# Performance work log

Hardware: AMD Instinct MI355X
Metric: run time of the kernel (lower is better)

The kernel has to match this reference:

```python
import jax, jax.numpy as jnp
import numpy as np


def setup_inputs() -> dict:
    key = jax.random.key(0)
    k1, k2 = jax.random.split(key)
    B, C, H, W = 8, 128, 96, 160
    x1 = jax.random.normal(k1, (B, C, H, W), dtype=jnp.float32)
    x2 = jax.random.normal(k2, (B, C, H, W), dtype=jnp.float32)
    return {"x1": x1, "x2": x2, "d": 4}


def reference(x1, x2, d):
    # x1, x2: (B, C, H, W); output: (B, (2d+1)^2, H, W)
    b, c, h, w = x1.shape
    x2p = jnp.pad(x2, ((0, 0), (0, 0), (d, d), (d, d)))
    # Loop over the small fixed (2d+1)^2 displacement set (81 for d=4);
    # each term is a channel-reduced elementwise product (shift-multiply-sum).
    corrs = [
        jnp.einsum("bchw,bchw->bhw", x1,
                   jax.lax.dynamic_slice(x2p, (0, 0, i, j), (b, c, h, w)))
        for i in range(2 * d + 1)
        for j in range(2 * d + 1)
    ]
    out = jnp.stack(corrs, axis=1)  # (B, (2d+1)^2, H, W)
    return out / c
```

## Files before the change

### kernel.cpp

```cpp
#include <hip/hip_runtime.h>
#include <stdint.h>
#include <stddef.h>

#define Bb 8
#define Cc 128
#define Hh 96
#define Ww 160
#define HW (Hh*Ww)
#define Kk 81

typedef __attribute__((ext_vector_type(8))) short short8;
typedef __attribute__((ext_vector_type(4))) float floatx4;
typedef __attribute__((ext_vector_type(4))) unsigned int uintx4;

__device__ __forceinline__ uint32_t bf16rne(float f) {
  uint32_t u = __float_as_uint(f);
  return (u + 0x7FFFu + ((u >> 16) & 1u)) >> 16;
}


#define TPX 32
__global__ __launch_bounds__(256)
void transpose_kernel(const float* __restrict__ x1, const float* __restrict__ x2,
                      ushort* __restrict__ x1t, ushort* __restrict__ x2t) {
  __shared__ float lds[TPX * 130];
  const int t   = threadIdx.x;
  const int b   = blockIdx.y;
  const int hw0 = blockIdx.x * TPX;
  const float* src = blockIdx.z ? x2 : x1;
  ushort*      dst = blockIdx.z ? x2t : x1t;

  const int p4 = t & 7;
  const int cb = t >> 3;
#pragma unroll
  for (int i = 0; i < 4; ++i) {
    const int c = cb + i * 32;
    floatx4 v = *(const floatx4*)&src[(size_t)(b * Cc + c) * HW + hw0 + p4 * 4];
#pragma unroll
    for (int jj = 0; jj < 4; ++jj)
      lds[(p4 * 4 + jj) * 130 + c] = v[jj];
  }
  __syncthreads();

  const int px = t >> 3;
#pragma unroll
  for (int i = 0; i < 2; ++i) {
    const int k = (t & 7) + 8 * i;
    const float* row = &lds[px * 130 + k * 8];
    uint32_t q0 = bf16rne(row[0]) | (bf16rne(row[1]) << 16);
    uint32_t q1 = bf16rne(row[2]) | (bf16rne(row[3]) << 16);
    uint32_t q2 = bf16rne(row[4]) | (bf16rne(row[5]) << 16);
    uint32_t q3 = bf16rne(row[6]) | (bf16rne(row[7]) << 16);
    *(uintx4*)&dst[((size_t)b * HW + hw0 + px) * Cc + k * 8] = (uintx4){q0, q1, q2, q3};
  }
}

__device__ __forceinline__ int clampi(int v, int lo, int hi) {
  return v < lo ? lo : (v > hi ? hi : v);
}

#define LOADRAW(dst, tt, ckc)                                                  \
  dst = *(const short8*)&base2c[rowoff##tt + (ckc) * 32];

#define ZSEL(v, tt)                                                            \
  v = (okw && (unsigned)(gh2b + (tt)) < (unsigned)Hh) ? v                      \
      : (short8){0, 0, 0, 0, 0, 0, 0, 0};

#define SBAR() __builtin_amdgcn_sched_barrier(0)

__global__ __launch_bounds__(256, 3)
void corr_t3_kernel(const ushort* __restrict__ x1t, const ushort* __restrict__ x2t,
                    float* __restrict__ out) {
  __shared__ float ldsOut[Kk * 66];

  const int tid  = threadIdx.x;
  const int flat = blockIdx.x;
  const int b  = flat & 7;
  const int j  = flat >> 3;
  const int by = j / 10;
  const int bx = j - by * 10;
  const int w0 = bx * 16;
  const int h0 = by * 4;

  const int lane = tid & 63;
  const int wv   = tid >> 6;
  const int vy = wv & 1, vx = wv >> 1;
  const int n = lane & 15, quad = lane >> 4;
  const int s = n >> 3, pw = n & 7;

  floatx4 acc[10];
#pragma unroll
  for (int t = 0; t < 10; ++t) acc[t] = (floatx4){0.f, 0.f, 0.f, 0.f};

  const int gw2  = w0 - 4 + 8 * vx + n;
  const bool okw = (unsigned)gw2 < (unsigned)Ww;
  const int gw2c = clampi(gw2, 0, Ww - 1);
  const int gh2b = h0 - 4 + 2 * vy;

  const ushort* base2c = x2t + ((long)b * HW + gw2c) * Cc + quad * 8;
  const ushort* base1  = x1t + ((long)b * HW + (long)(h0 + 2 * vy + s) * Ww
                                + (w0 + 8 * vx + pw)) * Cc + quad * 8;

  const long rowoff0 = (long)clampi(gh2b + 0, 0, Hh - 1) * (Ww * Cc);
  const long rowoff1 = (long)clampi(gh2b + 1, 0, Hh - 1) * (Ww * Cc);
  const long rowoff2 = (long)clampi(gh2b + 2, 0, Hh - 1) * (Ww * Cc);
  const long rowoff3 = (long)clampi(gh2b + 3, 0, Hh - 1) * (Ww * Cc);
  const long rowoff4 = (long)clampi(gh2b + 4, 0, Hh - 1) * (Ww * Cc);
  const long rowoff5 = (long)clampi(gh2b + 5, 0, Hh - 1) * (Ww * Cc);
  const long rowoff6 = (long)clampi(gh2b + 6, 0, Hh - 1) * (Ww * Cc);
  const long rowoff7 = (long)clampi(gh2b + 7, 0, Hh - 1) * (Ww * Cc);
  const long rowoff8 = (long)clampi(gh2b + 8, 0, Hh - 1) * (Ww * Cc);
  const long rowoff9 = (long)clampi(gh2b + 9, 0, Hh - 1) * (Ww * Cc);

  const short8 bf0 = *(const short8*)&base1[0 * 32];
  const short8 bf1 = *(const short8*)&base1[1 * 32];
  const short8 bf2 = *(const short8*)&base1[2 * 32];
  const short8 bf3 = *(const short8*)&base1[3 * 32];

  short8 aA0, aA1, aA2, aA3, aA4, aA5, aA6, aA7, aA8, aA9;
  short8 aB0, aB1, aB2, aB3, aB4, aB5, aB6, aB7, aB8, aB9;

  LOADRAW(aA0, 0, 0); LOADRAW(aA1, 1, 0); LOADRAW(aA2, 2, 0); LOADRAW(aA3, 3, 0);
  LOADRAW(aA4, 4, 0); LOADRAW(aA5, 5, 0); LOADRAW(aA6, 6, 0); LOADRAW(aA7, 7, 0);
  LOADRAW(aA8, 8, 0); LOADRAW(aA9, 9, 0);
  SBAR();
  LOADRAW(aB0, 0, 1); LOADRAW(aB1, 1, 1); LOADRAW(aB2, 2, 1); LOADRAW(aB3, 3, 1);
  LOADRAW(aB4, 4, 1); LOADRAW(aB5, 5, 1); LOADRAW(aB6, 6, 1); LOADRAW(aB7, 7, 1);
  LOADRAW(aB8, 8, 1); LOADRAW(aB9, 9, 1);
  SBAR();
  ZSEL(aA0, 0); ZSEL(aA1, 1); ZSEL(aA2, 2); ZSEL(aA3, 3); ZSEL(aA4, 4);
  ZSEL(aA5, 5); ZSEL(aA6, 6); ZSEL(aA7, 7); ZSEL(aA8, 8); ZSEL(aA9, 9);
  acc[0] = __builtin_amdgcn_mfma_f32_16x16x32_bf16(aA0, bf0, acc[0], 0, 0, 0);
  acc[1] = __builtin_amdgcn_mfma_f32_16x16x32_bf16(aA1, bf0, acc[1], 0, 0, 0);
  acc[2] = __builtin_amdgcn_mfma_f32_16x16x32_bf16(aA2, bf0, acc[2], 0, 0, 0);
  acc[3] = __builtin_amdgcn_mfma_f32_16x16x32_bf16(aA3, bf0, acc[3], 0, 0, 0);
  acc[4] = __builtin_amdgcn_mfma_f32_16x16x32_bf16(aA4, bf0, acc[4], 0, 0, 0);
  acc[5] = __builtin_amdgcn_mfma_f32_16x16x32_bf16(aA5, bf0, acc[5], 0, 0, 0);
  acc[6] = __builtin_amdgcn_mfma_f32_16x16x32_bf16(aA6, bf0, acc[6], 0, 0, 0);
  acc[7] = __builtin_amdgcn_mfma_f32_16x16x32_bf16(aA7, bf0, acc[7], 0, 0, 0);
  acc[8] = __builtin_amdgcn_mfma_f32_16x16x32_bf16(aA8, bf0, acc[8], 0, 0, 0);
  acc[9] = __builtin_amdgcn_mfma_f32_16x16x32_bf16(aA9, bf0, acc[9], 0, 0, 0);
  SBAR();
  LOADRAW(aA0, 0, 2); LOADRAW(aA1, 1, 2); LOADRAW(aA2, 2, 2); LOADRAW(aA3, 3, 2);
  LOADRAW(aA4, 4, 2); LOADRAW(aA5, 5, 2); LOADRAW(aA6, 6, 2); LOADRAW(aA7, 7, 2);
  LOADRAW(aA8, 8, 2); LOADRAW(aA9, 9, 2);
  SBAR();
  ZSEL(aB0, 0); ZSEL(aB1, 1); ZSEL(aB2, 2); ZSEL(aB3, 3); ZSEL(aB4, 4);
  ZSEL(aB5, 5); ZSEL(aB6, 6); ZSEL(aB7, 7); ZSEL(aB8, 8); ZSEL(aB9, 9);
  acc[0] = __builtin_amdgcn_mfma_f32_16x16x32_bf16(aB0, bf1, acc[0], 0, 0, 0);
  acc[1] = __builtin_amdgcn_mfma_f32_16x16x32_bf16(aB1, bf1, acc[1], 0, 0, 0);
  acc[2] = __builtin_amdgcn_mfma_f32_16x16x32_bf16(aB2, bf1, acc[2], 0, 0, 0);
  acc[3] = __builtin_amdgcn_mfma_f32_16x16x32_bf16(aB3, bf1, acc[3], 0, 0, 0);
  acc[4] = __builtin_amdgcn_mfma_f32_16x16x32_bf16(aB4, bf1, acc[4], 0, 0, 0);
  acc[5] = __builtin_amdgcn_mfma_f32_16x16x32_bf16(aB5, bf1, acc[5], 0, 0, 0);
  acc[6] = __builtin_amdgcn_mfma_f32_16x16x32_bf16(aB6, bf1, acc[6], 0, 0, 0);
  acc[7] = __builtin_amdgcn_mfma_f32_16x16x32_bf16(aB7, bf1, acc[7], 0, 0, 0);
  acc[8] = __builtin_amdgcn_mfma_f32_16x16x32_bf16(aB8, bf1, acc[8], 0, 0, 0);
  acc[9] = __builtin_amdgcn_mfma_f32_16x16x32_bf16(aB9, bf1, acc[9], 0, 0, 0);
  SBAR();
  LOADRAW(aB0, 0, 3); LOADRAW(aB1, 1, 3); LOADRAW(aB2, 2, 3); LOADRAW(aB3, 3, 3);
  LOADRAW(aB4, 4, 3); LOADRAW(aB5, 5, 3); LOADRAW(aB6, 6, 3); LOADRAW(aB7, 7, 3);
  LOADRAW(aB8, 8, 3); LOADRAW(aB9, 9, 3);
  SBAR();
  ZSEL(aA0, 0); ZSEL(aA1, 1); ZSEL(aA2, 2); ZSEL(aA3, 3); ZSEL(aA4, 4);
  ZSEL(aA5, 5); ZSEL(aA6, 6); ZSEL(aA7, 7); ZSEL(aA8, 8); ZSEL(aA9, 9);
  acc[0] = __builtin_amdgcn_mfma_f32_16x16x32_bf16(aA0, bf2, acc[0], 0, 0, 0);
  acc[1] = __builtin_amdgcn_mfma_f32_16x16x32_bf16(aA1, bf2, acc[1], 0, 0, 0);
  acc[2] = __builtin_amdgcn_mfma_f32_16x16x32_bf16(aA2, bf2, acc[2], 0, 0, 0);
  acc[3] = __builtin_amdgcn_mfma_f32_16x16x32_bf16(aA3, bf2, acc[3], 0, 0, 0);
  acc[4] = __builtin_amdgcn_mfma_f32_16x16x32_bf16(aA4, bf2, acc[4], 0, 0, 0);
  acc[5] = __builtin_amdgcn_mfma_f32_16x16x32_bf16(aA5, bf2, acc[5], 0, 0, 0);
  acc[6] = __builtin_amdgcn_mfma_f32_16x16x32_bf16(aA6, bf2, acc[6], 0, 0, 0);
  acc[7] = __builtin_amdgcn_mfma_f32_16x16x32_bf16(aA7, bf2, acc[7], 0, 0, 0);
  acc[8] = __builtin_amdgcn_mfma_f32_16x16x32_bf16(aA8, bf2, acc[8], 0, 0, 0);
  acc[9] = __builtin_amdgcn_mfma_f32_16x16x32_bf16(aA9, bf2, acc[9], 0, 0, 0);
  SBAR();
  ZSEL(aB0, 0); ZSEL(aB1, 1); ZSEL(aB2, 2); ZSEL(aB3, 3); ZSEL(aB4, 4);
  ZSEL(aB5, 5); ZSEL(aB6, 6); ZSEL(aB7, 7); ZSEL(aB8, 8); ZSEL(aB9, 9);
  acc[0] = __builtin_amdgcn_mfma_f32_16x16x32_bf16(aB0, bf3, acc[0], 0, 0, 0);
  acc[1] = __builtin_amdgcn_mfma_f32_16x16x32_bf16(aB1, bf3, acc[1], 0, 0, 0);
  acc[2] = __builtin_amdgcn_mfma_f32_16x16x32_bf16(aB2, bf3, acc[2], 0, 0, 0);
  acc[3] = __builtin_amdgcn_mfma_f32_16x16x32_bf16(aB3, bf3, acc[3], 0, 0, 0);
  acc[4] = __builtin_amdgcn_mfma_f32_16x16x32_bf16(aB4, bf3, acc[4], 0, 0, 0);
  acc[5] = __builtin_amdgcn_mfma_f32_16x16x32_bf16(aB5, bf3, acc[5], 0, 0, 0);
  acc[6] = __builtin_amdgcn_mfma_f32_16x16x32_bf16(aB6, bf3, acc[6], 0, 0, 0);
  acc[7] = __builtin_amdgcn_mfma_f32_16x16x32_bf16(aB7, bf3, acc[7], 0, 0, 0);
  acc[8] = __builtin_amdgcn_mfma_f32_16x16x32_bf16(aB8, bf3, acc[8], 0, 0, 0);
  acc[9] = __builtin_amdgcn_mfma_f32_16x16x32_bf16(aB9, bf3, acc[9], 0, 0, 0);

  const float scale = 1.0f / 128.0f;
  const int prow = 2 * vy + s;
  const int pcol = 8 * vx + pw;
#pragma unroll
  for (int t = 0; t < 10; ++t) {
    int di = t - 4 - s;
    if ((unsigned)(di + 4) > 8u) continue;
#pragma unroll
    for (int r = 0; r < 4; ++r) {
      int dj = quad * 4 + r - 4 - pw;
      if ((unsigned)(dj + 4) > 8u) continue;
      int kk = (di + 4) * 9 + (dj + 4);
      ldsOut[kk * 66 + prow * 16 + pcol] = acc[t][r] * scale;
    }
  }
  __syncthreads();

  for (int idx = tid; idx < Kk * 64; idx += 256) {
    int kk  = idx >> 6;
    int rem = idx & 63;
    int hh  = rem >> 4;
    int ww  = rem & 15;
    out[((size_t)b * Kk + kk) * HW + (size_t)(h0 + hh) * Ww + (w0 + ww)] =
        ldsOut[kk * 66 + rem];
  }
}

__global__ __launch_bounds__(512, 4)
void corr_kernel(const float* __restrict__ x1, const float* __restrict__ x2,
                 float* __restrict__ out) {
  __shared__ __align__(16) ushort ldsX2[16*24*40];
  __shared__ __align__(16) ushort ldsX1[8*16*40];

  const int tid = threadIdx.x;
  const int flat = blockIdx.x;
  const int b  = flat & 7;
  const int j  = flat >> 3;
  const int by = j / 10;
  const int bx = j - by * 10;
  const int w0 = bx * 16;
  const int h0 = by * 8;

  const int lane = tid & 63;
  const int wv   = tid >> 6;
  const int vy = wv & 3, vx = wv >> 2;
  const int n = lane & 15, quad = lane >> 4;
  const int s = n >> 3, pw = n & 7;

  floatx4 acc[10];
#pragma unroll
  for (int t = 0; t < 10; ++t) acc[t] = (floatx4){0.f, 0.f, 0.f, 0.f};

  for (int ck = 0; ck < 4; ++ck) {
    const int c0 = ck * 32;
    if (ck) __syncthreads();

#pragma unroll
    for (int it = 0; it < 3; ++it) {
      int T   = it * 512 + tid;
      int w24 = T % 24;
      int t2  = T / 24;
      int rw  = t2 & 15;
      int cg  = t2 >> 4;
      int gh = h0 - 4 + rw;
      int gw = w0 - 4 + w24;
      bool ok = ((unsigned)gh < Hh) && ((unsigned)gw < Ww);
      const float* src = x2 + ((size_t)(b*Cc + c0 + cg*8) * HW + gh*Ww + gw);
      uint32_t p0, p1, p2, p3;
      {
        float a0 = ok ? src[0*HW] : 0.f;
        float a1 = ok ? src[1*HW] : 0.f;
        float a2 = ok ? src[2*HW] : 0.f;
        float a3 = ok ? src[3*HW] : 0.f;
        float a4 = ok ? src[4*HW] : 0.f;
        float a5 = ok ? src[5*HW] : 0.f;
        float a6 = ok ? src[6*HW] : 0.f;
        float a7 = ok ? src[7*HW] : 0.f;
        p0 = bf16rne(a0) | (bf16rne(a1) << 16);
        p1 = bf16rne(a2) | (bf16rne(a3) << 16);
        p2 = bf16rne(a4) | (bf16rne(a5) << 16);
        p3 = bf16rne(a6) | (bf16rne(a7) << 16);
      }
      *(uintx4*)&ldsX2[(rw*24 + w24)*40 + cg*8] = (uintx4){p0, p1, p2, p3};
    }

    {
      int T  = tid;
      int wl = T & 15;
      int t2 = T >> 4;
      int rl = t2 & 7;
      int cg = t2 >> 3;
      const float* src = x1 + ((size_t)(b*Cc + c0 + cg*8) * HW
                               + (h0 + rl)*Ww + (w0 + wl));
      uint32_t p0, p1, p2, p3;
      float a0 = src[0*HW], a1 = src[1*HW], a2 = src[2*HW], a3 = src[3*HW];
      float a4 = src[4*HW], a5 = src[5*HW], a6 = src[6*HW], a7 = src[7*HW];
      p0 = bf16rne(a0) | (bf16rne(a1) << 16);
      p1 = bf16rne(a2) | (bf16rne(a3) << 16);
      p2 = bf16rne(a4) | (bf16rne(a5) << 16);
      p3 = bf16rne(a6) | (bf16rne(a7) << 16);
      *(uintx4*)&ldsX1[(rl*16 + wl)*40 + cg*8] = (uintx4){p0, p1, p2, p3};
    }

    __syncthreads();

    short8 bfrag = *(const short8*)&ldsX1[((2*vy + s)*16 + 8*vx + pw)*40 + quad*8];
#pragma unroll
    for (int t = 0; t < 10; ++t) {
      short8 afrag = *(const short8*)&ldsX2[((2*vy + t)*24 + 8*vx + n)*40 + quad*8];
      acc[t] = __builtin_amdgcn_mfma_f32_16x16x32_bf16(afrag, bfrag, acc[t], 0, 0, 0);
    }
  }

  const float scale = 1.0f / 128.0f;
  const int ph  = h0 + 2*vy + s;
  const int pwg = w0 + 8*vx + pw;
#pragma unroll
  for (int t = 0; t < 10; ++t) {
    int di = t - 4 - s;
    if ((unsigned)(di + 4) > 8u) continue;
#pragma unroll
    for (int r = 0; r < 4; ++r) {
      int dj = quad*4 + r - 4 - pw;
      if ((unsigned)(dj + 4) > 8u) continue;
      int kk = (di + 4) * 9 + (dj + 4);
      out[((size_t)b*Kk + kk) * HW + ph*Ww + pwg] = acc[t][r] * scale;
    }
  }
}

extern "C" void kernel_launch(void* const* d_in, const int* in_sizes, int n_in,
                              void* d_out, int out_size, void* d_ws, size_t ws_size,
                              hipStream_t stream) {
  const float* x1 = (const float*)d_in[0];
  const float* x2 = (const float*)d_in[1];
  float* out = (float*)d_out;

  const size_t elems = (size_t)Bb * HW * Cc;
  const size_t need  = 2 * elems * sizeof(ushort);

  if (d_ws != nullptr && ws_size >= need) {
    ushort* x1t = (ushort*)d_ws;
    ushort* x2t = x1t + elems;
    transpose_kernel<<<dim3(HW / TPX, Bb, 2), dim3(256, 1, 1), 0, stream>>>(
        x1, x2, x1t, x2t);
    corr_t3_kernel<<<dim3(1920, 1, 1), dim3(256, 1, 1), 0, stream>>>(x1t, x2t, out);
  } else {
    corr_kernel<<<dim3(960, 1, 1), dim3(512, 1, 1), 0, stream>>>(x1, x2, out);
  }
}
```

Measured before the change: 207.0 us.

## Software-pipeline transpose kernel over four tiles with double-buffered LDS

Each transpose block now handles four 32-pixel tiles instead of one. It uses two LDS buffers so the global loads for the next tile are issued while the current tile is scattered and drained. This is meant to hide global-load latency and cut block-launch overhead in the fp32-to-bf16 NHWC transpose pre-pass. In exchange the grid has a quarter as many blocks, LDS use per block doubles, and there are more barriers per block.

```diff
diff --git a/kernel.cpp b/kernel.cpp
--- a/kernel.cpp
+++ b/kernel.cpp
@@ -18,41 +18,86 @@
   return (u + 0x7FFFu + ((u >> 16) & 1u)) >> 16;
 }
 
+#define SBAR() __builtin_amdgcn_sched_barrier(0)
+
 
 #define TPX 32
-__global__ __launch_bounds__(256)
+__global__ __launch_bounds__(256, 4)
 void transpose_kernel(const float* __restrict__ x1, const float* __restrict__ x2,
                       ushort* __restrict__ x1t, ushort* __restrict__ x2t) {
-  __shared__ float lds[TPX * 130];
+  __shared__ float lds[2][TPX * 130];
   const int t   = threadIdx.x;
   const int b   = blockIdx.y;
-  const int hw0 = blockIdx.x * TPX;
   const float* src = blockIdx.z ? x2 : x1;
   ushort*      dst = blockIdx.z ? x2t : x1t;
+  const int tile0 = blockIdx.x * 4;
 
   const int p4 = t & 7;
   const int cb = t >> 3;
-#pragma unroll
-  for (int i = 0; i < 4; ++i) {
-    const int c = cb + i * 32;
-    floatx4 v = *(const floatx4*)&src[(size_t)(b * Cc + c) * HW + hw0 + p4 * 4];
-#pragma unroll
-    for (int jj = 0; jj < 4; ++jj)
-      lds[(p4 * 4 + jj) * 130 + c] = v[jj];
-  }
-  __syncthreads();
-
   const int px = t >> 3;
-#pragma unroll
-  for (int i = 0; i < 2; ++i) {
-    const int k = (t & 7) + 8 * i;
-    const float* row = &lds[px * 130 + k * 8];
-    uint32_t q0 = bf16rne(row[0]) | (bf16rne(row[1]) << 16);
-    uint32_t q1 = bf16rne(row[2]) | (bf16rne(row[3]) << 16);
-    uint32_t q2 = bf16rne(row[4]) | (bf16rne(row[5]) << 16);
-    uint32_t q3 = bf16rne(row[6]) | (bf16rne(row[7]) << 16);
-    *(uintx4*)&dst[((size_t)b * HW + hw0 + px) * Cc + k * 8] = (uintx4){q0, q1, q2, q3};
-  }
+  const int k0 = t & 7;
+
+  const float* chan = src + (size_t)(b * Cc + cb) * HW + p4 * 4;
+
+  floatx4 v0, v1, v2, v3;
+
+#define TLOAD(ti)                                                              \
+  {                                                                            \
+    const float* sb = chan + (size_t)(tile0 + (ti)) * TPX;                     \
+    v0 = *(const floatx4*)(sb + (size_t) 0 * HW);                              \
+    v1 = *(const floatx4*)(sb + (size_t)32 * HW);                              \
+    v2 = *(const floatx4*)(sb + (size_t)64 * HW);                              \
+    v3 = *(const floatx4*)(sb + (size_t)96 * HW);                              \
+  }
+
+#define TSCATTER(B)                                                            \
+  {                                                                            \
+    float* L = lds[B];                                                         \
+    _Pragma("unroll") for (int jj = 0; jj < 4; ++jj)                           \
+        L[(p4 * 4 + jj) * 130 + cb +  0] = v0[jj];                             \
+    _Pragma("unroll") for (int jj = 0; jj < 4; ++jj)                           \
+        L[(p4 * 4 + jj) * 130 + cb + 32] = v1[jj];                             \
+    _Pragma("unroll") for (int jj = 0; jj < 4; ++jj)                           \
+        L[(p4 * 4 + jj) * 130 + cb + 64] = v2[jj];                             \
+    _Pragma("unroll") for (int jj = 0; jj < 4; ++jj)                           \
+        L[(p4 * 4 + jj) * 130 + cb + 96] = v3[jj];                             \
+  }
+
+#define TDRAIN(ti, B)                                                          \
+  {                                                                            \
+    const float* rowa = &lds[B][px * 130 + k0 * 8];                            \
+    const float* rowb = &lds[B][px * 130 + (k0 + 8) * 8];                      \
+    float f0 = rowa[0], f1 = rowa[1], f2 = rowa[2], f3 = rowa[3];              \
+    float f4 = rowa[4], f5 = rowa[5], f6 = rowa[6], f7 = rowa[7];              \
+    float g0 = rowb[0], g1 = rowb[1], g2 = rowb[2], g3 = rowb[3];              \
+    float g4 = rowb[4], g5 = rowb[5], g6 = rowb[6], g7 = rowb[7];              \
+    uintx4 qa = (uintx4){bf16rne(f0) | (bf16rne(f1) << 16),                    \
+                         bf16rne(f2) | (bf16rne(f3) << 16),                    \
+                         bf16rne(f4) | (bf16rne(f5) << 16),                    \
+                         bf16rne(f6) | (bf16rne(f7) << 16)};                   \
+    uintx4 qb = (uintx4){bf16rne(g0) | (bf16rne(g1) << 16),                    \
+                         bf16rne(g2) | (bf16rne(g3) << 16),                    \
+                         bf16rne(g4) | (bf16rne(g5) << 16),                    \
+                         bf16rne(g6) | (bf16rne(g7) << 16)};                   \
+    ushort* dbase =                                                            \
+        &dst[((size_t)b * HW + (size_t)(tile0 + (ti)) * TPX + px) * Cc];       \
+    *(uintx4*)&dbase[k0 * 8]       = qa;                                       \
+    *(uintx4*)&dbase[(k0 + 8) * 8] = qb;                                       \
+  }
+
+  TLOAD(0);
+  TSCATTER(0); SBAR(); TLOAD(1); SBAR(); __syncthreads();
+  TDRAIN(0, 0); __syncthreads();
+  TSCATTER(1); SBAR(); TLOAD(2); SBAR(); __syncthreads();
+  TDRAIN(1, 1); __syncthreads();
+  TSCATTER(0); SBAR(); TLOAD(3); SBAR(); __syncthreads();
+  TDRAIN(2, 0); __syncthreads();
+  TSCATTER(1); __syncthreads();
+  TDRAIN(3, 1);
+
+#undef TLOAD
+#undef TSCATTER
+#undef TDRAIN
 }
 
 __device__ __forceinline__ int clampi(int v, int lo, int hi) {
@@ -65,8 +110,6 @@
 #define ZSEL(v, tt)                                                            \
   v = (okw && (unsigned)(gh2b + (tt)) < (unsigned)Hh) ? v                      \
       : (short8){0, 0, 0, 0, 0, 0, 0, 0};
-
-#define SBAR() __builtin_amdgcn_sched_barrier(0)
 
 __global__ __launch_bounds__(256, 3)
 void corr_t3_kernel(const ushort* __restrict__ x1t, const ushort* __restrict__ x2t,
@@ -331,7 +374,7 @@
   if (d_ws != nullptr && ws_size >= need) {
     ushort* x1t = (ushort*)d_ws;
     ushort* x2t = x1t + elems;
-    transpose_kernel<<<dim3(HW / TPX, Bb, 2), dim3(256, 1, 1), 0, stream>>>(
+    transpose_kernel<<<dim3(HW / (TPX * 4), Bb, 2), dim3(256, 1, 1), 0, stream>>>(
         x1, x2, x1t, x2t);
     corr_t3_kernel<<<dim3(1920, 1, 1), dim3(256, 1, 1), 0, stream>>>(x1t, x2t, out);
   } else {
```

Measured after the change: 205.9 us. No clear change (-0.5%).

## Switch bf16 intermediate layout to channel-group-major blocks of eight channels

Applied to the files above, without the earlier changes.

The transposed bf16 buffers go from [B][HW][128] to [B][16 groups][HW][8], so each pixel's 8-channel chunk is 16 bytes and the chunk groups are separated by a large stride. The transpose kernel now handles 512 pixels by 8 channels per block, with plain row copies into LDS and contiguous 16-byte stores. The correlation kernel's addressing is updated to match, so each MFMA operand load for neighbouring pixels reads contiguous memory within a group. The aim is cheaper transpose traffic and better-coalesced loads in the correlation kernel. The cost is that the K-chunk loads now jump a large stride apart.

```diff
diff --git a/kernel.cpp b/kernel.cpp
--- a/kernel.cpp
+++ b/kernel.cpp
@@ -18,40 +18,48 @@
   return (u + 0x7FFFu + ((u >> 16) & 1u)) >> 16;
 }
 
-
-#define TPX 32
-__global__ __launch_bounds__(256)
+#define SBAR() __builtin_amdgcn_sched_barrier(0)
+
+
+#define TPX3 512
+__global__ __launch_bounds__(256, 8)
 void transpose_kernel(const float* __restrict__ x1, const float* __restrict__ x2,
                       ushort* __restrict__ x1t, ushort* __restrict__ x2t) {
-  __shared__ float lds[TPX * 130];
+  __shared__ float lds[8][TPX3 + 4];
   const int t   = threadIdx.x;
   const int b   = blockIdx.y;
-  const int hw0 = blockIdx.x * TPX;
-  const float* src = blockIdx.z ? x2 : x1;
-  ushort*      dst = blockIdx.z ? x2t : x1t;
-
-  const int p4 = t & 7;
-  const int cb = t >> 3;
-#pragma unroll
-  for (int i = 0; i < 4; ++i) {
-    const int c = cb + i * 32;
-    floatx4 v = *(const floatx4*)&src[(size_t)(b * Cc + c) * HW + hw0 + p4 * 4];
-#pragma unroll
-    for (int jj = 0; jj < 4; ++jj)
-      lds[(p4 * 4 + jj) * 130 + c] = v[jj];
-  }
+  const int px0 = blockIdx.x * TPX3;
+  const int zz  = blockIdx.z;
+  const int cg  = zz & 15;
+  const float* src = (zz >> 4) ? x2 : x1;
+  ushort*      dst = (zz >> 4) ? x2t : x1t;
+
+  const int hi  = t >> 7;
+  const int pos = t & 127;
+  const float* sb = src + ((size_t)(b * Cc + cg * 8 + hi)) * HW + px0 + pos * 4;
+  floatx4 v0 = *(const floatx4*)(sb + (size_t)0 * HW);
+  floatx4 v1 = *(const floatx4*)(sb + (size_t)2 * HW);
+  floatx4 v2 = *(const floatx4*)(sb + (size_t)4 * HW);
+  floatx4 v3 = *(const floatx4*)(sb + (size_t)6 * HW);
+  SBAR();
+  *(floatx4*)&lds[0 + hi][pos * 4] = v0;
+  *(floatx4*)&lds[2 + hi][pos * 4] = v1;
+  *(floatx4*)&lds[4 + hi][pos * 4] = v2;
+  *(floatx4*)&lds[6 + hi][pos * 4] = v3;
+
   __syncthreads();
 
-  const int px = t >> 3;
-#pragma unroll
-  for (int i = 0; i < 2; ++i) {
-    const int k = (t & 7) + 8 * i;
-    const float* row = &lds[px * 130 + k * 8];
-    uint32_t q0 = bf16rne(row[0]) | (bf16rne(row[1]) << 16);
-    uint32_t q1 = bf16rne(row[2]) | (bf16rne(row[3]) << 16);
-    uint32_t q2 = bf16rne(row[4]) | (bf16rne(row[5]) << 16);
-    uint32_t q3 = bf16rne(row[6]) | (bf16rne(row[7]) << 16);
-    *(uintx4*)&dst[((size_t)b * HW + hw0 + px) * Cc + k * 8] = (uintx4){q0, q1, q2, q3};
+  ushort* dbase = dst + (((size_t)b * 16 + cg) * HW + px0) * 8;
+#pragma unroll
+  for (int j = 0; j < 2; ++j) {
+    const int px = j * 256 + t;
+    float c0 = lds[0][px], c1 = lds[1][px], c2 = lds[2][px], c3 = lds[3][px];
+    float c4 = lds[4][px], c5 = lds[5][px], c6 = lds[6][px], c7 = lds[7][px];
+    uintx4 q = (uintx4){bf16rne(c0) | (bf16rne(c1) << 16),
+                        bf16rne(c2) | (bf16rne(c3) << 16),
+                        bf16rne(c4) | (bf16rne(c5) << 16),
+                        bf16rne(c6) | (bf16rne(c7) << 16)};
+    *(uintx4*)&dbase[(size_t)px * 8] = q;
   }
 }
 
@@ -59,14 +67,14 @@
   return v < lo ? lo : (v > hi ? hi : v);
 }
 
+#define CKSTEP ((long)4 * HW * 8)
+
 #define LOADRAW(dst, tt, ckc)                                                  \
-  dst = *(const short8*)&base2c[rowoff##tt + (ckc) * 32];
+  dst = *(const short8*)&base2c[rowoff##tt + (ckc) * CKSTEP];
 
 #define ZSEL(v, tt)                                                            \
   v = (okw && (unsigned)(gh2b + (tt)) < (unsigned)Hh) ? v                      \
       : (short8){0, 0, 0, 0, 0, 0, 0, 0};
-
-#define SBAR() __builtin_amdgcn_sched_barrier(0)
 
 __global__ __launch_bounds__(256, 3)
 void corr_t3_kernel(const ushort* __restrict__ x1t, const ushort* __restrict__ x2t,
@@ -97,25 +105,26 @@
   const int gw2c = clampi(gw2, 0, Ww - 1);
   const int gh2b = h0 - 4 + 2 * vy;
 
-  const ushort* base2c = x2t + ((long)b * HW + gw2c) * Cc + quad * 8;
-  const ushort* base1  = x1t + ((long)b * HW + (long)(h0 + 2 * vy + s) * Ww
-                                + (w0 + 8 * vx + pw)) * Cc + quad * 8;
-
-  const long rowoff0 = (long)clampi(gh2b + 0, 0, Hh - 1) * (Ww * Cc);
-  const long rowoff1 = (long)clampi(gh2b + 1, 0, Hh - 1) * (Ww * Cc);
-  const long rowoff2 = (long)clampi(gh2b + 2, 0, Hh - 1) * (Ww * Cc);
-  const long rowoff3 = (long)clampi(gh2b + 3, 0, Hh - 1) * (Ww * Cc);
-  const long rowoff4 = (long)clampi(gh2b + 4, 0, Hh - 1) * (Ww * Cc);
-  const long rowoff5 = (long)clampi(gh2b + 5, 0, Hh - 1) * (Ww * Cc);
-  const long rowoff6 = (long)clampi(gh2b + 6, 0, Hh - 1) * (Ww * Cc);
-  const long rowoff7 = (long)clampi(gh2b + 7, 0, Hh - 1) * (Ww * Cc);
-  const long rowoff8 = (long)clampi(gh2b + 8, 0, Hh - 1) * (Ww * Cc);
-  const long rowoff9 = (long)clampi(gh2b + 9, 0, Hh - 1) * (Ww * Cc);
-
-  const short8 bf0 = *(const short8*)&base1[0 * 32];
-  const short8 bf1 = *(const short8*)&base1[1 * 32];
-  const short8 bf2 = *(const short8*)&base1[2 * 32];
-  const short8 bf3 = *(const short8*)&base1[3 * 32];
+  const ushort* base2c = x2t + (((long)b * 16 + quad) * HW + gw2c) * 8;
+  const ushort* base1  = x1t + (((long)b * 16 + quad) * HW
+                                + (long)(h0 + 2 * vy + s) * Ww
+                                + (w0 + 8 * vx + pw)) * 8;
+
+  const long rowoff0 = (long)clampi(gh2b + 0, 0, Hh - 1) * (Ww * 8);
+  const long rowoff1 = (long)clampi(gh2b + 1, 0, Hh - 1) * (Ww * 8);
+  const long rowoff2 = (long)clampi(gh2b + 2, 0, Hh - 1) * (Ww * 8);
+  const long rowoff3 = (long)clampi(gh2b + 3, 0, Hh - 1) * (Ww * 8);
+  const long rowoff4 = (long)clampi(gh2b + 4, 0, Hh - 1) * (Ww * 8);
+  const long rowoff5 = (long)clampi(gh2b + 5, 0, Hh - 1) * (Ww * 8);
+  const long rowoff6 = (long)clampi(gh2b + 6, 0, Hh - 1) * (Ww * 8);
+  const long rowoff7 = (long)clampi(gh2b + 7, 0, Hh - 1) * (Ww * 8);
+  const long rowoff8 = (long)clampi(gh2b + 8, 0, Hh - 1) * (Ww * 8);
+  const long rowoff9 = (long)clampi(gh2b + 9, 0, Hh - 1) * (Ww * 8);
+
+  const short8 bf0 = *(const short8*)&base1[0 * CKSTEP];
+  const short8 bf1 = *(const short8*)&base1[1 * CKSTEP];
+  const short8 bf2 = *(const short8*)&base1[2 * CKSTEP];
+  const short8 bf3 = *(const short8*)&base1[3 * CKSTEP];
 
   short8 aA0, aA1, aA2, aA3, aA4, aA5, aA6, aA7, aA8, aA9;
   short8 aB0, aB1, aB2, aB3, aB4, aB5, aB6, aB7, aB8, aB9;
@@ -331,7 +340,7 @@
   if (d_ws != nullptr && ws_size >= need) {
     ushort* x1t = (ushort*)d_ws;
     ushort* x2t = x1t + elems;
-    transpose_kernel<<<dim3(HW / TPX, Bb, 2), dim3(256, 1, 1), 0, stream>>>(
+    transpose_kernel<<<dim3(HW / TPX3, Bb, 32), dim3(256, 1, 1), 0, stream>>>(
         x1, x2, x1t, x2t);
     corr_t3_kernel<<<dim3(1920, 1, 1), dim3(256, 1, 1), 0, stream>>>(x1t, x2t, out);
   } else {
```

Measured after the change: 182.4 us, median of 2. 11.9% less time.
